# Optimization experiments

Measured on AMD Instinct MI355X. Metric: run time of the kernel, lower is better.

Reference implementation:

```python
import jax, jax.numpy as jnp
import numpy as np

N_EMBD = 1024
N_HEADS = 16
D_K = N_EMBD // N_HEADS


def setup_inputs() -> dict:
    key = jax.random.key(0)
    k1, k2, k3, k4, k5 = jax.random.split(key, 5)
    B, T, E = 4, 2048, N_EMBD
    scale = 1.0 / np.sqrt(E)
    inputs = jax.random.normal(k1, (B, T, E), dtype=jnp.float32)
    W_qkv = jax.random.normal(k2, (3 * E, E), dtype=jnp.float32) * scale
    b_qkv = jax.random.normal(k3, (3 * E,), dtype=jnp.float32) * 0.01
    W_out = jax.random.normal(k4, (E, E), dtype=jnp.float32) * scale
    b_out = jax.random.normal(k5, (E,), dtype=jnp.float32) * 0.01
    return {"inputs": inputs, "W_qkv": W_qkv, "b_qkv": b_qkv,
            "W_out": W_out, "b_out": b_out}


def reference(inputs, W_qkv, b_qkv, W_out, b_out):
    B, T, E = inputs.shape
    H, dk = N_HEADS, D_K
    # fused QKV projection: [B,T,3E]
    qkv = jnp.einsum('bte,fe->btf', inputs, W_qkv) + b_qkv
    # reshape to [B,T,H,3*dk] then to [B,H,T,3*dk], split into q,k,v
    qkv = qkv.reshape(B, T, H, 3 * dk).transpose(0, 2, 1, 3)
    q, k, v = jnp.split(qkv, 3, axis=-1)  # each [B,H,T,dk]
    scores = jnp.einsum('bhqd,bhkd->bhqk', q, k) / np.sqrt(dk)
    causal = jnp.tril(jnp.ones((T, T), dtype=bool))
    scores = jnp.where(causal, scores, -jnp.inf)
    attn = jax.nn.softmax(scores, axis=-1)
    out = jnp.einsum('bhqk,bhkd->bhqd', attn, v)  # [B,H,T,dk]
    out = out.transpose(0, 2, 1, 3).reshape(B, T, E)
    return jnp.einsum('bte,fe->btf', out, W_out) + b_out
```

## Files before the change

### kernel.cpp

```cpp
#include <hip/hip_runtime.h>
#include <stdint.h>


#define DEVFN static __device__ __forceinline__

typedef __attribute__((ext_vector_type(8))) __bf16 bf16x8;
typedef __attribute__((ext_vector_type(8))) ushort ushort8v;
typedef __attribute__((ext_vector_type(4))) float float4v;

#define AS1 __attribute__((address_space(1)))
#define AS3 __attribute__((address_space(3)))

DEVFN ushort f2bf(float f) {
  __bf16 h = (__bf16)f;
  union { __bf16 h; ushort u; } c; c.h = h;
  return c.u;
}

__global__ void cast3_f32_bf16(const float* __restrict__ a, int na,
                               const float* __restrict__ b, int nb,
                               const float* __restrict__ c, int nc,
                               ushort* __restrict__ out) {
  int total = na + nb + nc;
  int stride = gridDim.x * blockDim.x * 4;
  for (int j = (blockIdx.x * blockDim.x + threadIdx.x) * 4; j + 3 < total; j += stride) {
    const float* src;
    if (j < na) src = a + j;
    else if (j < na + nb) src = b + (j - na);
    else src = c + (j - na - nb);
    float4 v = *reinterpret_cast<const float4*>(src);
    ushort4 o;
    o.x = f2bf(v.x); o.y = f2bf(v.y); o.z = f2bf(v.z); o.w = f2bf(v.w);
    *reinterpret_cast<ushort4*>(out + j) = o;
  }
}

template<bool OUT_BF16, bool QSCALE>
__global__ __launch_bounds__(256) void gemm_bt(
    const ushort* __restrict__ A, const ushort* __restrict__ B,
    const float* __restrict__ bias, void* __restrict__ Cout,
    int M, int N, int K) {
  __shared__ ushort lds_a[128 * 32];
  __shared__ ushort lds_b[128 * 32];
  const int tid = threadIdx.x;
  const int lane = tid & 63;
  const int w = tid >> 6;
  const int wr = w >> 1, wc = w & 1;
  const int m0 = blockIdx.y * 128, n0 = blockIdx.x * 128;
  const int l15 = lane & 15, lg = lane >> 4;

  float4v acc[4][4] = {};

  for (int k0 = 0; k0 < K; k0 += 32) {
    __syncthreads();
#pragma unroll
    for (int it = 0; it < 2; ++it) {
      int idx = it * 256 + tid;
      int row = idx >> 2, ch = idx & 3;
      const ushort* ga = A + (size_t)(m0 + row) * K + k0 + ch * 8;
      const ushort* gb = B + (size_t)(n0 + row) * K + k0 + ch * 8;
      __builtin_amdgcn_global_load_lds((const AS1 uint32_t*)ga, (AS3 uint32_t*)&lds_a[idx * 8], 16, 0, 0);
      __builtin_amdgcn_global_load_lds((const AS1 uint32_t*)gb, (AS3 uint32_t*)&lds_b[idx * 8], 16, 0, 0);
    }
    __syncthreads();

    bf16x8 af[4], bfr[4];
#pragma unroll
    for (int m = 0; m < 4; ++m)
      af[m] = *reinterpret_cast<const bf16x8*>(&lds_a[(wr * 64 + m * 16 + l15) * 32 + lg * 8]);
#pragma unroll
    for (int n = 0; n < 4; ++n)
      bfr[n] = *reinterpret_cast<const bf16x8*>(&lds_b[(wc * 64 + n * 16 + l15) * 32 + lg * 8]);
#pragma unroll
    for (int m = 0; m < 4; ++m)
#pragma unroll
      for (int n = 0; n < 4; ++n)
        acc[m][n] = __builtin_amdgcn_mfma_f32_16x16x32_bf16(af[m], bfr[n], acc[m][n], 0, 0, 0);
  }

#pragma unroll
  for (int n = 0; n < 4; ++n) {
    int col = n0 + wc * 64 + n * 16 + l15;
    float bv = bias[col];
    float f = 1.0f;
    if (QSCALE && (((col >> 4) % 12) < 4)) f = 0.125f * 1.44269504f;
#pragma unroll
    for (int m = 0; m < 4; ++m) {
#pragma unroll
      for (int r = 0; r < 4; ++r) {
        int rowg = m0 + wr * 64 + m * 16 + lg * 4 + r;
        float vv = (acc[m][n][r] + bv) * f;
        if (OUT_BF16)
          ((ushort*)Cout)[(size_t)rowg * N + col] = f2bf(vv);
        else
          ((float*)Cout)[(size_t)rowg * N + col] = vv;
      }
    }
  }
}

__global__ __launch_bounds__(256) void transpose_v(
    const ushort* __restrict__ qkv, ushort* __restrict__ vt) {
  const int bh = blockIdx.y, b = bh >> 4, h = bh & 15;
  const int w = threadIdx.x >> 6, lane = threadIdx.x & 63;
  const int tc = lane >> 3, dc = lane & 7;
  const int t0 = blockIdx.x * 256 + w * 64 + tc * 8;

  const ushort* src = qkv + (size_t)(b * 2048 + t0) * 3072 + h * 192 + 128 + dc * 8;
  ushort r[8][8];
#pragma unroll
  for (int i = 0; i < 8; ++i) {
    ushort8v v = *reinterpret_cast<const ushort8v*>(src + (size_t)i * 3072);
#pragma unroll
    for (int j = 0; j < 8; ++j) r[i][j] = v[j];
  }
  ushort* dst = vt + ((size_t)bh * 64 + dc * 8) * 2048 + t0;
#pragma unroll
  for (int j = 0; j < 8; ++j) {
    ushort8v o;
#pragma unroll
    for (int i = 0; i < 8; ++i) o[i] = r[i][j];
    *reinterpret_cast<ushort8v*>(dst + (size_t)j * 2048) = o;
  }
}

__global__ __launch_bounds__(512, 6) void attn_kernel(
    const ushort* __restrict__ qkv, const ushort* __restrict__ vt,
    ushort* __restrict__ out) {
  __shared__ ushort k_lds[2][4096];
  __shared__ ushort v_lds[2][4096];
  __shared__ ushort p_lds[8][1024];

  const int qb = (int)gridDim.y - 1 - (int)blockIdx.y;
  const int bh = blockIdx.x;
  const int b = bh >> 4, h = bh & 15;
  const int tid = threadIdx.x, lane = tid & 63, w = tid >> 6;
  const int l15 = lane & 15, lg = lane >> 4;

  const size_t rs = 3072;
  const ushort* qbase = qkv + (size_t)(b * 2048) * rs + h * 192;
  const ushort* kbase = qbase + 64;
  const ushort* vtbase = vt + (size_t)bh * 64 * 2048;

  const int q0 = qb * 128;
  const int q0w = q0 + w * 16;
  const int nt = (qb + 1) * 2;

  bf16x8 qf[2];
#pragma unroll
  for (int kk = 0; kk < 2; ++kk)
    qf[kk] = *reinterpret_cast<const bf16x8*>(
        qbase + (size_t)(q0w + l15) * rs + kk * 32 + lg * 8);

  bf16x8 ones;
#pragma unroll
  for (int e = 0; e < 8; ++e) ones[e] = (__bf16)1.0f;

  const int srow = w * 8 + (lane >> 3);
  const int sch = (lane & 7) ^ ((lane >> 3) & 7);
  const ushort* ksrc = kbase + (size_t)srow * rs + sch * 8;
  const ushort* vsrc = vtbase + (size_t)srow * 2048 + sch * 8;
  const size_t kstep = (size_t)64 * rs;
  const size_t vstep = 64;

  __builtin_amdgcn_global_load_lds((const AS1 uint32_t*)ksrc, (AS3 uint32_t*)&k_lds[0][w * 512 + lane * 8], 16, 0, 0);
  __builtin_amdgcn_global_load_lds((const AS1 uint32_t*)vsrc, (AS3 uint32_t*)&v_lds[0][w * 512 + lane * 8], 16, 0, 0);
  ksrc += kstep; vsrc += vstep;
  __syncthreads();

  float4v oacc[4] = {};
  float4v lacc = {};

  int cur = 0;
  for (int t = 0; t < nt; ++t) {
    if (t + 1 < nt) {
      __builtin_amdgcn_global_load_lds((const AS1 uint32_t*)ksrc, (AS3 uint32_t*)&k_lds[cur ^ 1][w * 512 + lane * 8], 16, 0, 0);
      __builtin_amdgcn_global_load_lds((const AS1 uint32_t*)vsrc, (AS3 uint32_t*)&v_lds[cur ^ 1][w * 512 + lane * 8], 16, 0, 0);
      ksrc += kstep; vsrc += vstep;
    }

    if (t * 64 <= q0w + 15) {
      const ushort* kb = k_lds[cur];
      float4v s[4] = {};
      __builtin_amdgcn_s_setprio(1);
#pragma unroll
      for (int kk = 0; kk < 2; ++kk)
#pragma unroll
        for (int n = 0; n < 4; ++n) {
          int row = n * 16 + l15;
          bf16x8 kf = *reinterpret_cast<const bf16x8*>(&kb[row * 64 + (((kk * 4 + lg) ^ (row & 7)) * 8)]);
          s[n] = __builtin_amdgcn_mfma_f32_16x16x32_bf16(qf[kk], kf, s[n], 0, 0, 0);
        }
      __builtin_amdgcn_s_setprio(0);

      if (t * 64 + 63 > q0w) {
#pragma unroll
        for (int n = 0; n < 4; ++n) {
          int kvg = t * 64 + n * 16 + l15;
#pragma unroll
          for (int r = 0; r < 4; ++r) {
            int qg = q0w + lg * 4 + r;
            if (kvg > qg) s[n][r] = -1e30f;
          }
        }
      }

#pragma unroll
      for (int n = 0; n < 4; ++n) {
#pragma unroll
        for (int r = 0; r < 4; ++r) {
          float p = __builtin_amdgcn_exp2f(s[n][r]);
          int row = lg * 4 + r;
          int col = n * 16 + l15;
          int ch = (col >> 3) ^ (row & 7);
          p_lds[w][row * 64 + ch * 8 + (col & 7)] = f2bf(p);
        }
      }

      bf16x8 pf[2];
#pragma unroll
      for (int kk = 0; kk < 2; ++kk)
        pf[kk] = *reinterpret_cast<const bf16x8*>(&p_lds[w][l15 * 64 + (((kk * 4 + lg) ^ (l15 & 7)) * 8)]);

      const ushort* vb_ = v_lds[cur];
      __builtin_amdgcn_s_setprio(1);
#pragma unroll
      for (int kk = 0; kk < 2; ++kk) {
#pragma unroll
        for (int nd = 0; nd < 4; ++nd) {
          int vr = nd * 16 + l15;
          bf16x8 vf = *reinterpret_cast<const bf16x8*>(&vb_[vr * 64 + (((kk * 4 + lg) ^ (vr & 7)) * 8)]);
          oacc[nd] = __builtin_amdgcn_mfma_f32_16x16x32_bf16(pf[kk], vf, oacc[nd], 0, 0, 0);
        }
        lacc = __builtin_amdgcn_mfma_f32_16x16x32_bf16(pf[kk], ones, lacc, 0, 0, 0);
      }
      __builtin_amdgcn_s_setprio(0);
    }

    __syncthreads();
    cur ^= 1;
  }

#pragma unroll
  for (int nd = 0; nd < 4; ++nd) {
#pragma unroll
    for (int r = 0; r < 4; ++r) {
      int qg = q0 + w * 16 + lg * 4 + r;
      int col = h * 64 + nd * 16 + l15;
      out[(size_t)(b * 2048 + qg) * 1024 + col] = f2bf(oacc[nd][r] / lacc[r]);
    }
  }
}

extern "C" void kernel_launch(void* const* d_in, const int* in_sizes, int n_in,
                              void* d_out, int out_size, void* d_ws, size_t ws_size,
                              hipStream_t stream) {
  (void)in_sizes; (void)n_in; (void)out_size; (void)ws_size;
  const float* x      = (const float*)d_in[0];
  const float* w_qkv  = (const float*)d_in[1];
  const float* b_qkv  = (const float*)d_in[2];
  const float* w_out  = (const float*)d_in[3];
  const float* b_out  = (const float*)d_in[4];
  float* outp = (float*)d_out;

  const int BT = 4 * 2048;
  const int E = 1024, N3 = 3072;

  char* ws = (char*)d_ws;
  ushort* xb    = (ushort*)ws;  ws += (size_t)BT * E * 2;
  ushort* wqkvb = (ushort*)ws;  ws += (size_t)N3 * E * 2;
  ushort* woutb = (ushort*)ws;  ws += (size_t)E * E * 2;
  ushort* qkvb  = (ushort*)ws;  ws += (size_t)BT * N3 * 2;
  ushort* attb  = (ushort*)ws;  ws += (size_t)BT * E * 2;
  ushort* vtb   = xb;

  cast3_f32_bf16<<<2048, 256, 0, stream>>>(x, BT * E, w_qkv, N3 * E, w_out, E * E, xb);

  dim3 g1(N3 / 128, BT / 128);
  gemm_bt<true, true><<<g1, 256, 0, stream>>>(xb, wqkvb, b_qkv, qkvb, BT, N3, E);

  dim3 gt(8, 64);
  transpose_v<<<gt, 256, 0, stream>>>(qkvb, vtb);

  dim3 g2(64, 16);
  attn_kernel<<<g2, 512, 0, stream>>>(qkvb, vtb, attb);

  dim3 g3(E / 128, BT / 128);
  gemm_bt<false, false><<<g3, 256, 0, stream>>>(attb, woutb, b_out, outp, BT, E, E);
}
```

Before: 195.1 us.

## Double-buffer GEMM LDS tiles with swizzled layout and XCD-aware block remap

Rewrites the bf16 GEMM main loop to double-buffer the LDS tiles, so the next K-slice is fetched with global_load_lds while MFMAs run on the current one, and the loop needs one barrier per iteration instead of two. It also XOR-swizzles the 16-byte chunk placement in LDS to cut bank conflicts on fragment reads. Work-groups are remapped across the eight XCDs to improve L2 locality, and wave priority is raised around the MFMA block. The cost is double the LDS use, which may lower occupancy, and there is a risk of a race because a single barrier must cover both the async LDS fill and the reads of the other buffer.

```diff
diff --git a/kernel.cpp b/kernel.cpp
--- a/kernel.cpp
+++ b/kernel.cpp
@@ -40,43 +40,70 @@
     const ushort* __restrict__ A, const ushort* __restrict__ B,
     const float* __restrict__ bias, void* __restrict__ Cout,
     int M, int N, int K) {
-  __shared__ ushort lds_a[128 * 32];
-  __shared__ ushort lds_b[128 * 32];
+  __shared__ ushort lds_a[2][128 * 32];
+  __shared__ ushort lds_b[2][128 * 32];
   const int tid = threadIdx.x;
   const int lane = tid & 63;
   const int w = tid >> 6;
   const int wr = w >> 1, wc = w & 1;
-  const int m0 = blockIdx.y * 128, n0 = blockIdx.x * 128;
   const int l15 = lane & 15, lg = lane >> 4;
 
+  const int nwg = (int)(gridDim.x * gridDim.y);
+  const int orig = (int)(blockIdx.y * gridDim.x + blockIdx.x);
+  const int cpx = nwg >> 3;
+  const int swz = ((orig & 7) * cpx) + (orig >> 3);
+  const int bx = swz % (int)gridDim.x, by = swz / (int)gridDim.x;
+  const int m0 = by * 128, n0 = bx * 128;
+
+  const int srow = tid >> 2;
+  const int sch = tid & 3;
+  const int schs0 = sch ^ ((srow >> 1) & 3);
+  const int schs1 = sch ^ (((srow + 64) >> 1) & 3);
+  const ushort* ga0 = A + (size_t)(m0 + srow) * K + schs0 * 8;
+  const ushort* gb0 = B + (size_t)(n0 + srow) * K + schs0 * 8;
+  const ushort* ga1 = A + (size_t)(m0 + srow + 64) * K + schs1 * 8;
+  const ushort* gb1 = B + (size_t)(n0 + srow + 64) * K + schs1 * 8;
+
+#define STAGE(buf, k0)                                                                             \
+  {                                                                                                \
+    __builtin_amdgcn_global_load_lds((const AS1 uint32_t*)(ga0 + (k0)), (AS3 uint32_t*)&lds_a[buf][tid * 8], 16, 0, 0);        \
+    __builtin_amdgcn_global_load_lds((const AS1 uint32_t*)(gb0 + (k0)), (AS3 uint32_t*)&lds_b[buf][tid * 8], 16, 0, 0);        \
+    __builtin_amdgcn_global_load_lds((const AS1 uint32_t*)(ga1 + (k0)), (AS3 uint32_t*)&lds_a[buf][2048 + tid * 8], 16, 0, 0); \
+    __builtin_amdgcn_global_load_lds((const AS1 uint32_t*)(gb1 + (k0)), (AS3 uint32_t*)&lds_b[buf][2048 + tid * 8], 16, 0, 0); \
+  }
+
   float4v acc[4][4] = {};
 
+  STAGE(0, 0);
+  __syncthreads();
+
+  int cur = 0;
   for (int k0 = 0; k0 < K; k0 += 32) {
-    __syncthreads();
-#pragma unroll
-    for (int it = 0; it < 2; ++it) {
-      int idx = it * 256 + tid;
-      int row = idx >> 2, ch = idx & 3;
-      const ushort* ga = A + (size_t)(m0 + row) * K + k0 + ch * 8;
-      const ushort* gb = B + (size_t)(n0 + row) * K + k0 + ch * 8;
-      __builtin_amdgcn_global_load_lds((const AS1 uint32_t*)ga, (AS3 uint32_t*)&lds_a[idx * 8], 16, 0, 0);
-      __builtin_amdgcn_global_load_lds((const AS1 uint32_t*)gb, (AS3 uint32_t*)&lds_b[idx * 8], 16, 0, 0);
-    }
-    __syncthreads();
+    if (k0 + 32 < K) STAGE(cur ^ 1, k0 + 32);
 
     bf16x8 af[4], bfr[4];
 #pragma unroll
-    for (int m = 0; m < 4; ++m)
-      af[m] = *reinterpret_cast<const bf16x8*>(&lds_a[(wr * 64 + m * 16 + l15) * 32 + lg * 8]);
-#pragma unroll
-    for (int n = 0; n < 4; ++n)
-      bfr[n] = *reinterpret_cast<const bf16x8*>(&lds_b[(wc * 64 + n * 16 + l15) * 32 + lg * 8]);
+    for (int m = 0; m < 4; ++m) {
+      int row = wr * 64 + m * 16 + l15;
+      af[m] = *reinterpret_cast<const bf16x8*>(&lds_a[cur][row * 32 + ((lg ^ ((row >> 1) & 3)) * 8)]);
+    }
+#pragma unroll
+    for (int n = 0; n < 4; ++n) {
+      int row = wc * 64 + n * 16 + l15;
+      bfr[n] = *reinterpret_cast<const bf16x8*>(&lds_b[cur][row * 32 + ((lg ^ ((row >> 1) & 3)) * 8)]);
+    }
+    __builtin_amdgcn_s_setprio(1);
 #pragma unroll
     for (int m = 0; m < 4; ++m)
 #pragma unroll
       for (int n = 0; n < 4; ++n)
         acc[m][n] = __builtin_amdgcn_mfma_f32_16x16x32_bf16(af[m], bfr[n], acc[m][n], 0, 0, 0);
-  }
+    __builtin_amdgcn_s_setprio(0);
+
+    __syncthreads();
+    cur ^= 1;
+  }
+#undef STAGE
 
 #pragma unroll
   for (int n = 0; n < 4; ++n) {
```

Result: faster. 182.2 us (-6.6%).
